# Performance work log

Measured on AMD Instinct MI355X. Metric: run time of the kernel, lower is better.

The kernel has to match this reference:

```python
import jax, jax.numpy as jnp
import numpy as np

B, S, T, H, V = 32, 64, 64, 512, 32000


def setup_inputs() -> dict:
    key = jax.random.key(0)
    ks = jax.random.split(key, 14)
    enc = jax.random.normal(ks[0], (B, S, H), jnp.float32)
    h0 = jax.random.normal(ks[1], (1, B, H), jnp.float32)
    # encoder padding mask: at least half of each row valid (avoids all -inf rows)
    src_len = jax.random.randint(ks[2], (B,), S // 2, S + 1)
    enc_mask = (jnp.arange(S)[None, :] < src_len[:, None])
    tgt = jax.random.randint(ks[3], (B, T), 0, V)
    fra_len = jax.random.randint(ks[4], (B,), 1, T + 1).at[0].set(T)
    s = 1.0 / np.sqrt(H)
    emb = jax.random.normal(ks[5], (V, H), jnp.float32) * s
    W_ih = jax.random.uniform(ks[6], (3 * H, H), jnp.float32, -s, s)
    W_hh = jax.random.uniform(ks[7], (3 * H, H), jnp.float32, -s, s)
    b_ih = jax.random.uniform(ks[8], (3 * H,), jnp.float32, -s, s)
    b_hh = jax.random.uniform(ks[9], (3 * H,), jnp.float32, -s, s)
    W_cc = jax.random.uniform(ks[10], (H, 2 * H), jnp.float32, -s, s)
    b_cc = jnp.zeros((H,), jnp.float32)
    W_out = jax.random.uniform(ks[11], (V, H), jnp.float32, -s, s)
    b_out = jnp.zeros((V,), jnp.float32)
    return {"all_encoder_hidden_states": enc, "initial_decoder_hidden_state": h0,
            "encoder_output_mask": enc_mask, "target_input": tgt, "fra_length": fra_len,
            "embedding": emb, "W_ih": W_ih, "W_hh": W_hh, "b_ih": b_ih, "b_hh": b_hh,
            "W_cc": W_cc, "b_cc": b_cc, "W_out": W_out, "b_out": b_out}


def reference(all_encoder_hidden_states, initial_decoder_hidden_state, encoder_output_mask,
              target_input, fra_length, embedding, W_ih, W_hh, b_ih, b_hh,
              W_cc, b_cc, W_out, b_out):
    enc = all_encoder_hidden_states            # [B,S,H]
    mask = encoder_output_mask                 # [B,S] bool
    xs = embedding[target_input].transpose(1, 0, 2)  # [T,B,H]
    ts = jnp.arange(xs.shape[0])

    def step(h, inp):                          # h: [B,H]
        x, t = inp
        gx = x @ W_ih.T + b_ih                 # [B,3H]
        gh = h @ W_hh.T + b_hh
        gxr, gxz, gxn = jnp.split(gx, 3, axis=-1)
        ghr, ghz, ghn = jnp.split(gh, 3, axis=-1)
        r = jax.nn.sigmoid(gxr + ghr)
        z = jax.nn.sigmoid(gxz + ghz)
        n = jnp.tanh(gxn + r * ghn)
        h_new = (1.0 - z) * n + z * h          # torch GRU update
        # Luong dot-product attention
        scores = jnp.einsum('bsh,bh->bs', enc, h_new)
        scores = jnp.where(mask, scores, -jnp.inf)
        alphas = jax.nn.softmax(scores, axis=-1)
        ctx = jnp.einsum('bs,bsh->bh', alphas, enc)
        ho = jnp.tanh(jnp.concatenate([ctx, h_new], axis=-1) @ W_cc.T + b_cc)
        logit = ho @ W_out.T + b_out           # [B,V]
        active = (t < fra_length)[:, None]
        h_next = jnp.where(active, h_new, h)   # freeze finished sequences
        return h_next, logit

    _, logits = jax.lax.scan(step, initial_decoder_hidden_state[0], (xs, ts))
    logits = logits.transpose(1, 0, 2)          # [B,T,V]
    return jax.nn.log_softmax(logits, axis=-1)
```

## Files before the change

### kernel.cpp

```cpp
#include <hip/hip_runtime.h>

static constexpr int Bn = 32, Sn = 64, Tn = 64, Hn = 512, Vn = 32000;
static constexpr int H3 = 1536;
static constexpr int NBLK = 64;

typedef __attribute__((ext_vector_type(8))) short bf16x8;
typedef __attribute__((ext_vector_type(4))) float f32x4;

__device__ __forceinline__ short f2bf(float f) {
    unsigned u = __float_as_uint(f);
    u += 0x7FFFu + ((u >> 16) & 1u);
    return (short)(u >> 16);
}
__device__ __forceinline__ float bf2f(short s) {
    return __uint_as_float(((unsigned)(unsigned short)s) << 16);
}

__device__ __forceinline__ void gload16(const void* g, void* l) {
    __builtin_amdgcn_global_load_lds(
        (const __attribute__((address_space(1))) unsigned int*)g,
        (__attribute__((address_space(3))) unsigned int*)l, 16, 0, 0);
}

__global__ __launch_bounds__(128) void k_gather(const int* __restrict__ tgt,
                                                const float* __restrict__ emb,
                                                short* __restrict__ Xb) {
    int m = blockIdx.x;
    int c = threadIdx.x * 4;
    const float4 v = *(const float4*)(emb + (long)tgt[m] * Hn + c);
    short4 o; o.x = f2bf(v.x); o.y = f2bf(v.y); o.z = f2bf(v.z); o.w = f2bf(v.w);
    *(short4*)(Xb + (long)m * Hn + c) = o;
}

__global__ __launch_bounds__(256) void k_cvt(const float* __restrict__ src, int src_ld, int src_off,
                                             short* __restrict__ dst, long total4) {
    for (long i = (long)blockIdx.x * 256 + threadIdx.x; i < total4; i += (long)gridDim.x * 256) {
        long e = i * 4;
        long r = e >> 9; int c = (int)(e & 511);
        const float4 v = *(const float4*)(src + r * (long)src_ld + src_off + c);
        short4 o; o.x = f2bf(v.x); o.y = f2bf(v.y); o.z = f2bf(v.z); o.w = f2bf(v.w);
        *(short4*)(dst + e) = o;
    }
}

__global__ __launch_bounds__(256) void k_gemm_bf16(const short* __restrict__ A, int lda,
                                                   const short* __restrict__ Bm, int ldb,
                                                   const float* __restrict__ bias,
                                                   float* __restrict__ C, int ldc, int K) {
    __shared__ short lA[4096];
    __shared__ short lB[4096];
    const int tid = threadIdx.x;
    const int row0 = blockIdx.y * 128;
    const int col0 = blockIdx.x * 128;
    const int lane = tid & 63;
    const int w = tid >> 6;
    const int wr = w >> 1, wc = w & 1;
    const int g = lane >> 4, rr = lane & 15;

    f32x4 acc[4][4];
    for (int m = 0; m < 4; ++m)
        for (int n = 0; n < 4; ++n)
            for (int q = 0; q < 4; ++q) acc[m][n][q] = 0.f;

    for (int kk = 0; kk < K; kk += 32) {
        for (int p = 0; p < 2; ++p) {
            int u = p * 256 + tid;
            int kg = u >> 7, r = u & 127;
            gload16(A + (long)(row0 + r) * lda + kk + kg * 8, &lA[u * 8]);
            gload16(Bm + (long)(col0 + r) * ldb + kk + kg * 8, &lB[u * 8]);
        }
        __syncthreads();
        bf16x8 av[4], bv[4];
        for (int m = 0; m < 4; ++m)
            av[m] = *(const bf16x8*)&lA[(g * 128 + wr * 64 + m * 16 + rr) * 8];
        for (int n = 0; n < 4; ++n)
            bv[n] = *(const bf16x8*)&lB[(g * 128 + wc * 64 + n * 16 + rr) * 8];
        for (int m = 0; m < 4; ++m)
            for (int n = 0; n < 4; ++n)
                acc[m][n] = __builtin_amdgcn_mfma_f32_16x16x32_bf16(av[m], bv[n], acc[m][n], 0, 0, 0);
        __syncthreads();
    }

    for (int n = 0; n < 4; ++n) {
        int gc = col0 + wc * 64 + n * 16 + rr;
        float bb = bias ? bias[gc] : 0.f;
        for (int m = 0; m < 4; ++m) {
            int gr = row0 + wr * 64 + m * 16 + g * 4;
            for (int q = 0; q < 4; ++q)
                C[(long)(gr + q) * ldc + gc] = acc[m][n][q] + bb;
        }
    }
}

struct WSm2 {
    short h_all[Bn * Hn];
    short hnb[2][Bn * Hn];
    float gh_sl[3 * 16 * 32];
    float y1l[Bn * 16];
    int   flen[Bn];
};
struct BSm2 {
    short encl[Sn * 520];
    short encWl[Sn * Hn];
    float scp[8][64];
    float al[64];
    short hnf[Hn];
};
union USm2 { WSm2 w; BSm2 b; };

__device__ __forceinline__ void sig_flag(unsigned* slot, unsigned val) {
    asm volatile("s_waitcnt vmcnt(0)" ::: "memory");
    __syncthreads();
    if (threadIdx.x == 0)
        __hip_atomic_store(slot, val, __ATOMIC_RELAXED, __HIP_MEMORY_SCOPE_AGENT);
}
__device__ __forceinline__ void wait_flags32(const unsigned* base, unsigned need) {
    if (threadIdx.x < 32) {
        while (__hip_atomic_load(base + threadIdx.x * 32, __ATOMIC_RELAXED, __HIP_MEMORY_SCOPE_AGENT) < need)
            __builtin_amdgcn_s_sleep(1);
    }
    __syncthreads();
}

__global__ __launch_bounds__(512, 1) void k_seq(
    const float* __restrict__ GX, const float* __restrict__ enc,
    const void* __restrict__ maskp, const int* __restrict__ fra,
    const float* __restrict__ h0,
    const short* __restrict__ Whh_b, const float* __restrict__ b_hh,
    const short* __restrict__ Wcc2_b, const float* __restrict__ b_cc,
    const float* __restrict__ encW,
    short* __restrict__ ho_out,
    unsigned long long* __restrict__ hn_pub,
    float* __restrict__ y1_pub,
    unsigned* __restrict__ flags)
{
    __shared__ __align__(16) USm2 sm;
    const int bid = blockIdx.x;
    const int tid = threadIdx.x;
    const int wv = tid >> 6, lane = tid & 63;
    unsigned* flagW = flags;
    unsigned* flagB = flags + 1024;

    if (bid < Bn) {
        bf16x8 afr[16];
        if (wv < 6) {
            const int g = wv >> 1;
            const int row = g * 512 + bid * 16 + (lane & 15);
            #pragma unroll
            for (int k = 0; k < 16; ++k)
                afr[k] = *(const bf16x8*)(Whh_b + (long)row * 512 + k * 32 + (lane >> 4) * 8);
        } else {
            const int row = bid * 16 + (lane & 15);
            #pragma unroll
            for (int k = 0; k < 16; ++k)
                afr[k] = *(const bf16x8*)(Wcc2_b + (long)row * 512 + k * 32 + (lane >> 4) * 8);
        }
        if (tid < Bn) sm.w.flen[tid] = fra[tid];
        #pragma unroll
        for (int it = 0; it < 8; ++it) {
            const int idx2 = it * 512 + tid;
            const int b = idx2 >> 7, ci2 = idx2 & 127;
            const int j0 = ci2 * 4;
            const int soff = b * 512 + ((((ci2 >> 1)) ^ (b & 7)) << 3) + (ci2 & 1) * 4;
            const float4 v = *(const float4*)(h0 + b * 512 + j0);
            unsigned long long pk = (unsigned long long)(unsigned short)f2bf(v.x)
                                  | ((unsigned long long)(unsigned short)f2bf(v.y) << 16)
                                  | ((unsigned long long)(unsigned short)f2bf(v.z) << 32)
                                  | ((unsigned long long)(unsigned short)f2bf(v.w) << 48);
            *(unsigned long long*)&sm.w.h_all[soff] = pk;
        }

        const int eb = tid >> 4, jj = tid & 15;
        float h_carry = h0[eb * 512 + bid * 16 + jj];
        const int flen_e = fra[eb];

        for (int t = 0; t <= Tn + 1; ++t) {
            float gxr = 0.f, gxz = 0.f, gxn = 0.f;
            if (t < Tn) {
                const long base = (long)(eb * Tn + t) * H3 + bid * 16 + jj;
                gxr = GX[base]; gxz = GX[base + 512]; gxn = GX[base + 1024];
            }
            if (t >= 1 && t <= Tn) {
                wait_flags32(flagW, (unsigned)t);
                const unsigned long long* src = hn_pub + ((t - 1) & 1) * 4096;
                short* dst = sm.w.hnb[(t - 1) & 1];
                #pragma unroll
                for (int it = 0; it < 8; ++it) {
                    const int idx2 = it * 512 + tid;
                    const int b = idx2 >> 7, ci2 = idx2 & 127;
                    const int soff = b * 512 + ((((ci2 >> 1)) ^ (b & 7)) << 3) + (ci2 & 1) * 4;
                    const unsigned long long v = __hip_atomic_load(src + idx2, __ATOMIC_RELAXED, __HIP_MEMORY_SCOPE_AGENT);
                    *(unsigned long long*)&dst[soff] = v;
                    if (t - 1 < sm.w.flen[b]) *(unsigned long long*)&sm.w.h_all[soff] = v;
                }
            }
            if (t >= 2) {
                wait_flags32(flagB, (unsigned)(t - 1));
                sm.w.y1l[tid] = __hip_atomic_load(
                    y1_pub + ((t - 2) & 1) * (Bn * Hn) + (tid >> 4) * 512 + bid * 16 + (tid & 15),
                    __ATOMIC_RELAXED, __HIP_MEMORY_SCOPE_AGENT);
            }
            __syncthreads();
            if (t < Tn && wv < 6) {
                const int g = wv >> 1, n = wv & 1;
                const int bq = n * 16 + (lane & 15);
                f32x4 acc = {0.f, 0.f, 0.f, 0.f};
                #pragma unroll
                for (int k = 0; k < 16; ++k) {
                    const int c = k * 4 + (lane >> 4);
                    bf16x8 bfr = *(const bf16x8*)&sm.w.h_all[bq * 512 + ((c ^ (bq & 7)) << 3)];
                    acc = __builtin_amdgcn_mfma_f32_16x16x32_bf16(afr[k], bfr, acc, 0, 0, 0);
                }
                const int r0 = (lane >> 4) * 4;
                #pragma unroll
                for (int q = 0; q < 4; ++q)
                    sm.w.gh_sl[g * 512 + (r0 + q) * 32 + bq] = acc[q];
            }
            if (t >= 2 && wv >= 6) {
                const int n = wv - 6;
                const int bq = n * 16 + (lane & 15);
                const short* hsrc = sm.w.hnb[(t - 2) & 1];
                f32x4 acc = {0.f, 0.f, 0.f, 0.f};
                #pragma unroll
                for (int k = 0; k < 16; ++k) {
                    const int c = k * 4 + (lane >> 4);
                    bf16x8 bfr = *(const bf16x8*)&hsrc[bq * 512 + ((c ^ (bq & 7)) << 3)];
                    acc = __builtin_amdgcn_mfma_f32_16x16x32_bf16(afr[k], bfr, acc, 0, 0, 0);
                }
                const int r0 = (lane >> 4) * 4;
                short4 o;
                o.x = f2bf(tanhf(acc[0] + sm.w.y1l[bq * 16 + r0 + 0] + b_cc[bid * 16 + r0 + 0]));
                o.y = f2bf(tanhf(acc[1] + sm.w.y1l[bq * 16 + r0 + 1] + b_cc[bid * 16 + r0 + 1]));
                o.z = f2bf(tanhf(acc[2] + sm.w.y1l[bq * 16 + r0 + 2] + b_cc[bid * 16 + r0 + 2]));
                o.w = f2bf(tanhf(acc[3] + sm.w.y1l[bq * 16 + r0 + 3] + b_cc[bid * 16 + r0 + 3]));
                *(short4*)(ho_out + ((long)(bq * Tn + (t - 2))) * Hn + bid * 16 + r0) = o;
            }
            __syncthreads();
            if (t < Tn) {
                const int j = bid * 16 + jj;
                const float ghr = sm.w.gh_sl[jj * 32 + eb]          + b_hh[j];
                const float ghz = sm.w.gh_sl[512 + jj * 32 + eb]    + b_hh[512 + j];
                const float ghn = sm.w.gh_sl[1024 + jj * 32 + eb]   + b_hh[1024 + j];
                const float r = 1.f / (1.f + expf(-(gxr + ghr)));
                const float z = 1.f / (1.f + expf(-(gxz + ghz)));
                const float nn = tanhf(gxn + r * ghn);
                const float hv = (1.f - z) * nn + z * h_carry;
                h_carry = (t < flen_e) ? hv : h_carry;
                int w32 = (int)(unsigned short)f2bf(hv);
                int n1 = __shfl_down(w32, 1);
                int n2 = __shfl_down(w32, 2);
                int n3 = __shfl_down(w32, 3);
                if ((jj & 3) == 0) {
                    unsigned long long pk = (unsigned long long)(unsigned)(w32 | (n1 << 16))
                                          | ((unsigned long long)(unsigned)(n2 | (n3 << 16)) << 32);
                    __hip_atomic_store(hn_pub + (t & 1) * 4096 + eb * 128 + bid * 4 + (jj >> 2), pk,
                                       __ATOMIC_RELAXED, __HIP_MEMORY_SCOPE_AGENT);
                }
                sig_flag(flagW + bid * 32, (unsigned)(t + 1));
            }
        }
    } else {
        const int b = bid - Bn;
        const unsigned w0 = ((const unsigned*)maskp)[0];
        const int mmode = (w0 == 1u) ? 0 : (w0 == 0x3F800000u ? 2 : 1);
        {
            const float* encb = enc + (long)b * (Sn * Hn);
            #pragma unroll
            for (int it = 0; it < 16; ++it) {
                int e = (it * 512 + tid) * 4;
                float4 v = *(const float4*)(encb + e);
                int s = e >> 9, k = e & 511;
                short4 o; o.x = f2bf(v.x); o.y = f2bf(v.y); o.z = f2bf(v.z); o.w = f2bf(v.w);
                *(short4*)(sm.b.encl + s * 520 + k) = o;
            }
        }
        {
            const float* ewb = encW + (long)b * (Sn * Hn);
            #pragma unroll
            for (int it = 0; it < 16; ++it) {
                int e = (it * 512 + tid) * 4;
                float4 v = *(const float4*)(ewb + e);
                short4 o; o.x = f2bf(v.x); o.y = f2bf(v.y); o.z = f2bf(v.z); o.w = f2bf(v.w);
                *(short4*)(sm.b.encWl + e) = o;
            }
        }

        for (int u = 0; u < Tn; ++u) {
            wait_flags32(flagW, (unsigned)(u + 1));
            if (tid < 128) {
                unsigned long long v = __hip_atomic_load(hn_pub + (u & 1) * 4096 + b * 128 + tid,
                                                         __ATOMIC_RELAXED, __HIP_MEMORY_SCOPE_AGENT);
                *(unsigned long long*)&sm.b.hnf[tid * 4] = v;
            }
            __syncthreads();
            {
                const int s = tid & 63, sub = tid >> 6;
                const short* erow = sm.b.encl + s * 520 + sub * 64;
                const short* hrow = sm.b.hnf + sub * 64;
                float p = 0.f;
                #pragma unroll
                for (int c8 = 0; c8 < 8; ++c8) {
                    bf16x8 ev = *(const bf16x8*)(erow + c8 * 8);
                    bf16x8 hv8 = *(const bf16x8*)(hrow + c8 * 8);
                    #pragma unroll
                    for (int e = 0; e < 8; ++e)
                        p += bf2f(ev[e]) * bf2f(hv8[e]);
                }
                sm.b.scp[sub][s] = p;
            }
            __syncthreads();
            if (tid < 64) {
                float v = 0.f;
                #pragma unroll
                for (int q = 0; q < 8; ++q) v += sm.b.scp[q][tid];
                bool mv;
                if (mmode == 0)      mv = ((const int*)maskp)[b * Sn + tid] != 0;
                else if (mmode == 1) mv = ((const unsigned char*)maskp)[b * Sn + tid] != 0;
                else                 mv = ((const float*)maskp)[b * Sn + tid] != 0.f;
                v = mv ? v : -__builtin_inff();
                float mx = v;
                for (int o = 1; o < 64; o <<= 1) mx = fmaxf(mx, __shfl_xor(mx, o));
                float e = expf(v - mx);
                float su = e;
                for (int o = 1; o < 64; o <<= 1) su += __shfl_xor(su, o);
                sm.b.al[tid] = e / su;
            }
            __syncthreads();
            {
                float acc = 0.f;
                #pragma unroll 8
                for (int s = 0; s < 64; ++s)
                    acc += sm.b.al[s] * bf2f(sm.b.encWl[s * 512 + tid]);
                __hip_atomic_store(y1_pub + (u & 1) * (Bn * Hn) + b * 512 + tid, acc,
                                   __ATOMIC_RELAXED, __HIP_MEMORY_SCOPE_AGENT);
            }
            sig_flag(flagB + b * 32, (unsigned)(u + 1));
        }
    }
}

__global__ __launch_bounds__(256) void k_logsoftmax(float* __restrict__ out) {
    const long row = blockIdx.x;
    float* p = out + row * (long)Vn;
    const int tid = threadIdx.x;
    __shared__ float redm[4];
    __shared__ float reds[4];

    float mx = -__builtin_inff(), sm = 0.f;
    for (int i = tid; i < Vn / 4; i += 256) {
        float4 v = *(const float4*)(p + i * 4);
        float e0 = v.x, e1 = v.y, e2 = v.z, e3 = v.w;
        float m01 = fmaxf(e0, e1), m23 = fmaxf(e2, e3);
        float ml = fmaxf(m01, m23);
        float nm = fmaxf(mx, ml);
        sm = sm * __expf(mx - nm) + __expf(e0 - nm) + __expf(e1 - nm) + __expf(e2 - nm) + __expf(e3 - nm);
        mx = nm;
    }
    for (int o = 1; o < 64; o <<= 1) {
        float omx = __shfl_xor(mx, o), osm = __shfl_xor(sm, o);
        float nm = fmaxf(mx, omx);
        sm = sm * __expf(mx - nm) + osm * __expf(omx - nm);
        mx = nm;
    }
    if ((tid & 63) == 0) { redm[tid >> 6] = mx; reds[tid >> 6] = sm; }
    __syncthreads();
    float gmx = fmaxf(fmaxf(redm[0], redm[1]), fmaxf(redm[2], redm[3]));
    float gsm = reds[0] * __expf(redm[0] - gmx) + reds[1] * __expf(redm[1] - gmx)
              + reds[2] * __expf(redm[2] - gmx) + reds[3] * __expf(redm[3] - gmx);
    const float lse = gmx + logf(gsm);

    for (int i = tid; i < Vn / 4; i += 256) {
        float4 v = *(const float4*)(p + i * 4);
        v.x -= lse; v.y -= lse; v.z -= lse; v.w -= lse;
        *(float4*)(p + i * 4) = v;
    }
}

extern "C" void kernel_launch(void* const* d_in, const int* in_sizes, int n_in,
                              void* d_out, int out_size, void* d_ws, size_t ws_size,
                              hipStream_t stream) {
    const float* enc   = (const float*)d_in[0];
    const float* h0    = (const float*)d_in[1];
    const void*  maskp = d_in[2];
    const int*   tgt   = (const int*)d_in[3];
    const int*   fra   = (const int*)d_in[4];
    const float* emb   = (const float*)d_in[5];
    const float* W_ih  = (const float*)d_in[6];
    const float* W_hh  = (const float*)d_in[7];
    const float* b_ih  = (const float*)d_in[8];
    const float* b_hh  = (const float*)d_in[9];
    const float* W_cc  = (const float*)d_in[10];
    const float* b_cc  = (const float*)d_in[11];
    const float* W_out = (const float*)d_in[12];
    const float* b_out = (const float*)d_in[13];
    float* out = (float*)d_out;

    char* ws = (char*)d_ws;
    float*    GX      = (float*)ws;   ws += (long)2048 * 1536 * 4;
    float*    encW_ws = (float*)ws;   ws += (long)2048 * 512 * 4;
    short*    Xb      = (short*)ws;   ws += (long)2048 * 512 * 2;
    short*    Wih_b   = (short*)ws;   ws += (long)1536 * 512 * 2;
    short*    Wout_b  = (short*)ws;   ws += (long)32000 * 512 * 2;
    short*    Whh_b   = (short*)ws;   ws += (long)1536 * 512 * 2;
    short*    Wc1_b   = (short*)ws;   ws += (long)512 * 512 * 2;
    short*    Wcc2_b  = (short*)ws;   ws += (long)512 * 512 * 2;
    short*    enc_b   = (short*)ws;   ws += (long)2048 * 512 * 2;
    short*    ho_b    = (short*)ws;   ws += (long)2048 * 512 * 2;
    unsigned long long* hn_pub = (unsigned long long*)ws; ws += (long)2 * 4096 * 8;
    float*    y1_pub  = (float*)ws;   ws += (long)2 * 32 * 512 * 4;
    unsigned* flags   = (unsigned*)ws; ws += 2 * 1024 * 4;

    k_gather<<<2048, 128, 0, stream>>>(tgt, emb, Xb);
    k_cvt<<<768, 256, 0, stream>>>(W_ih, 512, 0, Wih_b, (long)1536 * 512 / 4);
    k_cvt<<<4096, 256, 0, stream>>>(W_out, 512, 0, Wout_b, (long)32000 * 512 / 4);
    k_cvt<<<768, 256, 0, stream>>>(W_hh, 512, 0, Whh_b, (long)1536 * 512 / 4);
    k_cvt<<<256, 256, 0, stream>>>(W_cc, 1024, 0, Wc1_b, (long)512 * 512 / 4);
    k_cvt<<<256, 256, 0, stream>>>(W_cc, 1024, 512, Wcc2_b, (long)512 * 512 / 4);
    k_cvt<<<1024, 256, 0, stream>>>(enc, 512, 0, enc_b, (long)2048 * 512 / 4);

    k_gemm_bf16<<<dim3(12, 16), 256, 0, stream>>>(Xb, 512, Wih_b, 512, b_ih, GX, 1536, 512);
    k_gemm_bf16<<<dim3(4, 16), 256, 0, stream>>>(enc_b, 512, Wc1_b, 512, nullptr, encW_ws, 512, 512);

    hipMemsetAsync(flags, 0, 2 * 1024 * 4, stream);
    k_seq<<<NBLK, 512, 0, stream>>>(GX, enc, maskp, fra, h0,
                                    Whh_b, b_hh, Wcc2_b, b_cc, encW_ws,
                                    ho_b, hn_pub, y1_pub, flags);

    k_gemm_bf16<<<dim3(250, 16), 256, 0, stream>>>(ho_b, 512, Wout_b, 512, b_out, out, 32000, 512);

    k_logsoftmax<<<2048, 256, 0, stream>>>(out);
}
```

Measured before the change: 754.5 us.

## Move attention-output wait off the GRU critical path and triple-buffer y1

The wait on the attention blocks' y1 flag and the ho projection are moved after the GRU update and h publication. The recurrent step is then no longer stalled by the attention pipeline. y1_pub gets a third buffer so producers can run further ahead without overwriting unread data. Both MFMA loops split their accumulation across two independent accumulators for more instruction-level parallelism. The cost is an extra __syncthreads per step and a three-slot buffer indexed with modulo arithmetic.

```diff
diff --git a/kernel.cpp b/kernel.cpp
--- a/kernel.cpp
+++ b/kernel.cpp
@@ -194,46 +194,24 @@
                     if (t - 1 < sm.w.flen[b]) *(unsigned long long*)&sm.w.h_all[soff] = v;
                 }
             }
-            if (t >= 2) {
-                wait_flags32(flagB, (unsigned)(t - 1));
-                sm.w.y1l[tid] = __hip_atomic_load(
-                    y1_pub + ((t - 2) & 1) * (Bn * Hn) + (tid >> 4) * 512 + bid * 16 + (tid & 15),
-                    __ATOMIC_RELAXED, __HIP_MEMORY_SCOPE_AGENT);
-            }
             __syncthreads();
             if (t < Tn && wv < 6) {
                 const int g = wv >> 1, n = wv & 1;
                 const int bq = n * 16 + (lane & 15);
-                f32x4 acc = {0.f, 0.f, 0.f, 0.f};
+                f32x4 a0 = {0.f, 0.f, 0.f, 0.f}, a1 = {0.f, 0.f, 0.f, 0.f};
                 #pragma unroll
-                for (int k = 0; k < 16; ++k) {
-                    const int c = k * 4 + (lane >> 4);
-                    bf16x8 bfr = *(const bf16x8*)&sm.w.h_all[bq * 512 + ((c ^ (bq & 7)) << 3)];
-                    acc = __builtin_amdgcn_mfma_f32_16x16x32_bf16(afr[k], bfr, acc, 0, 0, 0);
+                for (int k = 0; k < 8; ++k) {
+                    const int c0 = k * 4 + (lane >> 4);
+                    const int c1 = (k + 8) * 4 + (lane >> 4);
+                    bf16x8 b0 = *(const bf16x8*)&sm.w.h_all[bq * 512 + ((c0 ^ (bq & 7)) << 3)];
+                    bf16x8 b1 = *(const bf16x8*)&sm.w.h_all[bq * 512 + ((c1 ^ (bq & 7)) << 3)];
+                    a0 = __builtin_amdgcn_mfma_f32_16x16x32_bf16(afr[k], b0, a0, 0, 0, 0);
+                    a1 = __builtin_amdgcn_mfma_f32_16x16x32_bf16(afr[k + 8], b1, a1, 0, 0, 0);
                 }
                 const int r0 = (lane >> 4) * 4;
                 #pragma unroll
                 for (int q = 0; q < 4; ++q)
-                    sm.w.gh_sl[g * 512 + (r0 + q) * 32 + bq] = acc[q];
-            }
-            if (t >= 2 && wv >= 6) {
-                const int n = wv - 6;
-                const int bq = n * 16 + (lane & 15);
-                const short* hsrc = sm.w.hnb[(t - 2) & 1];
-                f32x4 acc = {0.f, 0.f, 0.f, 0.f};
-                #pragma unroll
-                for (int k = 0; k < 16; ++k) {
-                    const int c = k * 4 + (lane >> 4);
-                    bf16x8 bfr = *(const bf16x8*)&hsrc[bq * 512 + ((c ^ (bq & 7)) << 3)];
-                    acc = __builtin_amdgcn_mfma_f32_16x16x32_bf16(afr[k], bfr, acc, 0, 0, 0);
-                }
-                const int r0 = (lane >> 4) * 4;
-                short4 o;
-                o.x = f2bf(tanhf(acc[0] + sm.w.y1l[bq * 16 + r0 + 0] + b_cc[bid * 16 + r0 + 0]));
-                o.y = f2bf(tanhf(acc[1] + sm.w.y1l[bq * 16 + r0 + 1] + b_cc[bid * 16 + r0 + 1]));
-                o.z = f2bf(tanhf(acc[2] + sm.w.y1l[bq * 16 + r0 + 2] + b_cc[bid * 16 + r0 + 2]));
-                o.w = f2bf(tanhf(acc[3] + sm.w.y1l[bq * 16 + r0 + 3] + b_cc[bid * 16 + r0 + 3]));
-                *(short4*)(ho_out + ((long)(bq * Tn + (t - 2))) * Hn + bid * 16 + r0) = o;
+                    sm.w.gh_sl[g * 512 + (r0 + q) * 32 + bq] = a0[q] + a1[q];
             }
             __syncthreads();
             if (t < Tn) {
@@ -258,6 +236,35 @@
                 }
                 sig_flag(flagW + bid * 32, (unsigned)(t + 1));
             }
+            if (t >= 2) {
+                wait_flags32(flagB, (unsigned)(t - 1));
+                sm.w.y1l[tid] = __hip_atomic_load(
+                    y1_pub + ((t - 2) % 3) * (Bn * Hn) + (tid >> 4) * 512 + bid * 16 + (tid & 15),
+                    __ATOMIC_RELAXED, __HIP_MEMORY_SCOPE_AGENT);
+                __syncthreads();
+                if (wv >= 6) {
+                    const int n = wv - 6;
+                    const int bq = n * 16 + (lane & 15);
+                    const short* hsrc = sm.w.hnb[(t - 2) & 1];
+                    f32x4 a0 = {0.f, 0.f, 0.f, 0.f}, a1 = {0.f, 0.f, 0.f, 0.f};
+                    #pragma unroll
+                    for (int k = 0; k < 8; ++k) {
+                        const int c0 = k * 4 + (lane >> 4);
+                        const int c1 = (k + 8) * 4 + (lane >> 4);
+                        bf16x8 b0 = *(const bf16x8*)&hsrc[bq * 512 + ((c0 ^ (bq & 7)) << 3)];
+                        bf16x8 b1 = *(const bf16x8*)&hsrc[bq * 512 + ((c1 ^ (bq & 7)) << 3)];
+                        a0 = __builtin_amdgcn_mfma_f32_16x16x32_bf16(afr[k], b0, a0, 0, 0, 0);
+                        a1 = __builtin_amdgcn_mfma_f32_16x16x32_bf16(afr[k + 8], b1, a1, 0, 0, 0);
+                    }
+                    const int r0 = (lane >> 4) * 4;
+                    short4 o;
+                    o.x = f2bf(tanhf(a0[0] + a1[0] + sm.w.y1l[bq * 16 + r0 + 0] + b_cc[bid * 16 + r0 + 0]));
+                    o.y = f2bf(tanhf(a0[1] + a1[1] + sm.w.y1l[bq * 16 + r0 + 1] + b_cc[bid * 16 + r0 + 1]));
+                    o.z = f2bf(tanhf(a0[2] + a1[2] + sm.w.y1l[bq * 16 + r0 + 2] + b_cc[bid * 16 + r0 + 2]));
+                    o.w = f2bf(tanhf(a0[3] + a1[3] + sm.w.y1l[bq * 16 + r0 + 3] + b_cc[bid * 16 + r0 + 3]));
+                    *(short4*)(ho_out + ((long)(bq * Tn + (t - 2))) * Hn + bid * 16 + r0) = o;
+                }
+            }
         }
     } else {
         const int b = bid - Bn;
@@ -331,7 +338,7 @@
                 #pragma unroll 8
                 for (int s = 0; s < 64; ++s)
                     acc += sm.b.al[s] * bf2f(sm.b.encWl[s * 512 + tid]);
-                __hip_atomic_store(y1_pub + (u & 1) * (Bn * Hn) + b * 512 + tid, acc,
+                __hip_atomic_store(y1_pub + (u % 3) * (Bn * Hn) + b * 512 + tid, acc,
                                    __ATOMIC_RELAXED, __HIP_MEMORY_SCOPE_AGENT);
             }
             sig_flag(flagB + b * 32, (unsigned)(u + 1));
@@ -407,7 +414,7 @@
     short*    enc_b   = (short*)ws;   ws += (long)2048 * 512 * 2;
     short*    ho_b    = (short*)ws;   ws += (long)2048 * 512 * 2;
     unsigned long long* hn_pub = (unsigned long long*)ws; ws += (long)2 * 4096 * 8;
-    float*    y1_pub  = (float*)ws;   ws += (long)2 * 32 * 512 * 4;
+    float*    y1_pub  = (float*)ws;   ws += (long)3 * 32 * 512 * 4;
     unsigned* flags   = (unsigned*)ws; ws += 2 * 1024 * 4;
 
     k_gather<<<2048, 128, 0, stream>>>(tgt, emb, Xb);
```

Measured after the change: 751.0 us. Within noise of the previous version (-0.5%).
